# Kernel optimization log

Measured on AMD Instinct MI355X. Metric: run time of the kernel, lower is better.

Reference implementation:

```python
import jax, jax.numpy as jnp
import numpy as np

TAU = 2.0
EPS = 1e-5
SG_ALPHA = 4.0  # spikingjelly default Sigmoid surrogate alpha


@jax.custom_vjp
def heaviside(x):
    return (x >= 0.0).astype(x.dtype)

def _heaviside_fwd(x):
    return heaviside(x), x

def _heaviside_bwd(x, g):
    s = jax.nn.sigmoid(SG_ALPHA * x)
    return (g * SG_ALPHA * s * (1.0 - s),)

heaviside.defvjp(_heaviside_fwd, _heaviside_bwd)


def lif(x_seq, v_th):
    """Multi-step LIF, hard reset to 0, detach_reset=True. x_seq: (T, ...)."""
    def step(v, x_t):
        v = v + (x_t - v) / TAU
        s = heaviside(v - v_th)
        v = v * (1.0 - jax.lax.stop_gradient(s))  # detached hard reset
        return v, s
    _, spikes = jax.lax.scan(step, jnp.zeros_like(x_seq[0]), x_seq)
    return spikes


def bn(y, gamma, beta, mean, var):
    # y: (T, B, C, N); inference-mode BatchNorm1d over channel dim
    inv = gamma / jnp.sqrt(var + EPS)
    return y * inv[None, None, :, None] + (beta - mean * inv)[None, None, :, None]


def setup_inputs() -> dict:
    key = jax.random.key(0)
    ks = jax.random.split(key, 8)
    T, B, C, H, W = 4, 32, 256, 32, 32
    d = {
        "x": jax.random.normal(ks[0], (T, B, C, H, W), jnp.float32),
        "q_w": jax.random.normal(ks[1], (C, C), jnp.float32) * (1.0 / np.sqrt(C)),
        "q_gamma": jnp.ones((C,), jnp.float32),
        "q_beta": jnp.zeros((C,), jnp.float32),
        "q_mean": jnp.zeros((C,), jnp.float32),
        "q_var": jnp.ones((C,), jnp.float32),
        "k_w": jax.random.normal(ks[2], (C, C), jnp.float32) * (1.0 / np.sqrt(C)),
        "k_gamma": jnp.ones((C,), jnp.float32),
        "k_beta": jnp.zeros((C,), jnp.float32),
        "k_mean": jnp.zeros((C,), jnp.float32),
        "k_var": jnp.ones((C,), jnp.float32),
        "p_w": jax.random.normal(ks[3], (C, C), jnp.float32) * (1.0 / np.sqrt(C)),
        "p_b": jnp.zeros((C,), jnp.float32),
        "p_gamma": jnp.ones((C,), jnp.float32),
        "p_beta": jnp.zeros((C,), jnp.float32),
        "p_mean": jnp.zeros((C,), jnp.float32),
        "p_var": jnp.ones((C,), jnp.float32),
    }
    return d


def reference(x, q_w, q_gamma, q_beta, q_mean, q_var,
              k_w, k_gamma, k_beta, k_mean, k_var,
              p_w, p_b, p_gamma, p_beta, p_mean, p_var):
    T, B, C, H, W = x.shape
    num_heads = 8
    dh = C // num_heads
    N = H * W
    xs = x.reshape(T, B, C, N)

    # Q branch: 1x1 conv (C x C matmul) -> BN -> LIF
    q = bn(jnp.einsum('oc,tbcn->tbon', q_w, xs), q_gamma, q_beta, q_mean, q_var)
    q_spikes = lif(q, 1.0)                                # (T,B,C,N)
    q_h = q_spikes.reshape(T, B, num_heads, dh, N)

    # K branch
    k = bn(jnp.einsum('oc,tbcn->tbon', k_w, xs), k_gamma, k_beta, k_mean, k_var)
    k_spikes = lif(k, 1.0)
    k_h = k_spikes.reshape(T, B, num_heads, dh, N)

    # channel-sum pooled Q per head -> attn LIF (v_th=0.5) -> elementwise mult with K
    q_sum = jnp.sum(q_h, axis=3, keepdims=True)           # (T,B,h,1,N)
    attn = lif(q_sum, 0.5)
    x_one = attn * k_h                                    # (T,B,h,dh,N)

    # projection: 1x1 conv with bias -> BN -> LIF
    xo = x_one.reshape(T, B, C, N)
    xo = jnp.einsum('oc,tbcn->tbon', p_w, xo) + p_b[None, None, :, None]
    xo = bn(xo, p_gamma, p_beta, p_mean, p_var).reshape(T, B, C, H, W)
    x_final = lif(xo, 1.0)
    return x_final
```

## Files before the change

kernel.cpp:

```cpp
#include <hip/hip_runtime.h>
#include <cstdint>
#include <cstddef>

#define T_DIM 4
#define B_DIM 32
#define C_DIM 256
#define N_DIM 1024
#define NHEAD 8
#define DHEAD 32
#define NWRD 32

__device__ __forceinline__ float lif_step(float& v, float x, float vth) {
    v = __fadd_rn(v, __fmul_rn(__fsub_rn(x, v), 0.5f));
    const float s = (v >= vth) ? 1.0f : 0.0f;
    if (s != 0.0f) v = 0.0f;
    return s;
}

__device__ __forceinline__ void async_copy16(const float* g, float* l) {
    __builtin_amdgcn_global_load_lds(
        (const __attribute__((address_space(1))) unsigned int*)g,
        (__attribute__((address_space(3))) unsigned int*)l, 16, 0, 0);
}

__global__ __launch_bounds__(256) void k_transpose(
    const float* __restrict__ qw, const float* __restrict__ kw,
    const float* __restrict__ pw, float* __restrict__ wqk_t,
    float* __restrict__ p_t)
{
    const int i = blockIdx.x * 256 + threadIdx.x;
    if (i < C_DIM * 512) {
        const int k = i >> 9, col = i & 511;
        const int h = col >> 6, j = col & 63;
        wqk_t[i] = (j < 32) ? qw[(size_t)(h * 32 + j) * C_DIM + k]
                            : kw[(size_t)(h * 32 + j - 32) * C_DIM + k];
    } else {
        const int i2 = i - C_DIM * 512;
        const int k = i2 >> 8, c = i2 & 255;
        p_t[i2] = pw[(size_t)c * C_DIM + k];
    }
}

__global__ __launch_bounds__(256) void k_qk(
    const float* __restrict__ x, const float* __restrict__ wqk,
    const float* __restrict__ qg, const float* __restrict__ qbeta,
    const float* __restrict__ qmean, const float* __restrict__ qvar,
    const float* __restrict__ kg, const float* __restrict__ kbeta,
    const float* __restrict__ kmean, const float* __restrict__ kvar,
    uint32_t* __restrict__ xbits)
{
    __shared__ float w_lds[64 * 64];
    __shared__ float x_lds[64 * 64];
    __shared__ float qsum_lds[64];
    __shared__ float attn_lds[64];
    __shared__ uint32_t pack_lds[64];

    const int tid = threadIdx.x;
    const int h = blockIdx.x, nt = blockIdx.y, b = blockIdx.z;
    const int n0g = nt * 64;

    const int  mg   = tid >> 4;
    const int  m0   = mg << 2;
    const int  n0   = (tid & 15) << 2;
    const bool is_q = (mg < 8);

    float inv4[4], bias4[4];
    {
        const float* g  = is_q ? qg    : kg;
        const float* be = is_q ? qbeta : kbeta;
        const float* me = is_q ? qmean : kmean;
        const float* va = is_q ? qvar  : kvar;
        const int cb = h * DHEAD + (is_q ? m0 : (m0 - 32));
        #pragma unroll
        for (int i = 0; i < 4; i++) {
            const float iv = __fdiv_rn(g[cb + i], __fsqrt_rn(__fadd_rn(va[cb + i], 1e-5f)));
            inv4[i]  = iv;
            bias4[i] = __fsub_rn(be[cb + i], __fmul_rn(me[cb + i], iv));
        }
    }

    const int wid  = tid >> 6, lane = tid & 63;
    const int lr   = lane >> 4;
    const int lc   = (lane & 15) << 2;
    const int rbase = wid * 16;

    float* wl_dst = w_lds + rbase * 64;
    float* xl_dst = x_lds + rbase * 64;
    const float* wg0 = wqk + (size_t)(rbase + lr) * 512 + h * 64 + lc;

    float vstate[16];
    #pragma unroll
    for (int i = 0; i < 16; i++) vstate[i] = 0.0f;
    float v_attn = 0.0f;

    for (int t = 0; t < T_DIM; ++t) {
        float acc[16];
        #pragma unroll
        for (int i = 0; i < 16; i++) acc[i] = 0.0f;

        const float* xg0 = x + ((size_t)(t * B_DIM + b) * C_DIM + rbase + lr) * N_DIM + n0g + lc;

        for (int kk = 0; kk < C_DIM; kk += 64) {
            #pragma unroll
            for (int i = 0; i < 4; i++) {
                async_copy16(wg0 + (size_t)(kk + i * 4) * 512,   wl_dst + i * 256);
                async_copy16(xg0 + (size_t)(kk + i * 4) * N_DIM, xl_dst + i * 256);
            }
            __syncthreads();
            #pragma unroll 4
            for (int k = 0; k < 64; k++) {
                const float4 a  = *(const float4*)(w_lds + k * 64 + m0);
                const float4 bv = *(const float4*)(x_lds + k * 64 + n0);
                acc[ 0] = fmaf(a.x, bv.x, acc[ 0]);
                acc[ 1] = fmaf(a.x, bv.y, acc[ 1]);
                acc[ 2] = fmaf(a.x, bv.z, acc[ 2]);
                acc[ 3] = fmaf(a.x, bv.w, acc[ 3]);
                acc[ 4] = fmaf(a.y, bv.x, acc[ 4]);
                acc[ 5] = fmaf(a.y, bv.y, acc[ 5]);
                acc[ 6] = fmaf(a.y, bv.z, acc[ 6]);
                acc[ 7] = fmaf(a.y, bv.w, acc[ 7]);
                acc[ 8] = fmaf(a.z, bv.x, acc[ 8]);
                acc[ 9] = fmaf(a.z, bv.y, acc[ 9]);
                acc[10] = fmaf(a.z, bv.z, acc[10]);
                acc[11] = fmaf(a.z, bv.w, acc[11]);
                acc[12] = fmaf(a.w, bv.x, acc[12]);
                acc[13] = fmaf(a.w, bv.y, acc[13]);
                acc[14] = fmaf(a.w, bv.z, acc[14]);
                acc[15] = fmaf(a.w, bv.w, acc[15]);
            }
            __syncthreads();
        }

        float sarr[16];
        #pragma unroll
        for (int i = 0; i < 4; i++) {
            #pragma unroll
            for (int j = 0; j < 4; j++) {
                const float y = __fadd_rn(__fmul_rn(acc[i * 4 + j], inv4[i]), bias4[i]);
                sarr[i * 4 + j] = lif_step(vstate[i * 4 + j], y, 1.0f);
            }
        }

        if (tid < 64) { qsum_lds[tid] = 0.0f; pack_lds[tid] = 0u; }
        __syncthreads();

        if (is_q) {
            #pragma unroll
            for (int j = 0; j < 4; j++) {
                const float cs = sarr[j] + sarr[4 + j] + sarr[8 + j] + sarr[12 + j];
                atomicAdd(&qsum_lds[n0 + j], cs);
            }
        }
        __syncthreads();
        if (tid < 64) attn_lds[tid] = lif_step(v_attn, qsum_lds[tid], 0.5f);
        __syncthreads();

        if (!is_q) {
            #pragma unroll
            for (int i = 0; i < 4; i++) {
                uint32_t nib = 0;
                #pragma unroll
                for (int j = 0; j < 4; j++) {
                    if (sarr[i * 4 + j] != 0.0f && attn_lds[n0 + j] != 0.0f)
                        nib |= (1u << j);
                }
                if (nib)
                    atomicOr(&pack_lds[((m0 - 32) + i) * 2 + (n0 >> 5)], nib << (n0 & 31));
            }
        }
        __syncthreads();
        if (tid < 64) {
            const int row = tid >> 1, word = tid & 1;
            const int c = h * DHEAD + row;
            xbits[((size_t)(t * B_DIM + b) * C_DIM + c) * NWRD + (n0g >> 5) + word] = pack_lds[tid];
        }
    }
}

__global__ __launch_bounds__(256) void k_proj(
    const uint32_t* __restrict__ xbits, const float* __restrict__ pt,
    const float* __restrict__ pbias, const float* __restrict__ pg,
    const float* __restrict__ pbeta, const float* __restrict__ pmean,
    const float* __restrict__ pvar, float* __restrict__ out)
{
    __shared__ float w_lds[64 * 64];
    __shared__ float x_lds[64 * 64];

    const int tid = threadIdx.x;
    const int mt = blockIdx.x, nt = blockIdx.y, b = blockIdx.z;
    const int n0g = nt * 64;
    const int c0  = mt * 64;

    const int mg = tid >> 4, m0 = mg << 2;
    const int n0 = (tid & 15) << 2;

    float inv4[4], bias4[4], pb4[4];
    #pragma unroll
    for (int i = 0; i < 4; i++) {
        const int c = c0 + m0 + i;
        const float iv = __fdiv_rn(pg[c], __fsqrt_rn(__fadd_rn(pvar[c], 1e-5f)));
        inv4[i]  = iv;
        bias4[i] = __fsub_rn(pbeta[c], __fmul_rn(pmean[c], iv));
        pb4[i]   = pbias[c];
    }

    const int wid = tid >> 6, lane = tid & 63;
    const int lr  = lane >> 4;
    const int lc  = (lane & 15) << 2;
    const int rbase = wid * 16;

    float* wl_dst = w_lds + rbase * 64;
    const float* wg0 = pt + (size_t)(rbase + lr) * 256 + c0 + lc;
    const int wsel = (lane & 15) >> 3;
    const int shf  = (lane & 7) * 4;

    float vstate[16];
    #pragma unroll
    for (int i = 0; i < 16; i++) vstate[i] = 0.0f;

    for (int t = 0; t < T_DIM; ++t) {
        float acc[16];
        #pragma unroll
        for (int i = 0; i < 16; i++) acc[i] = 0.0f;

        const uint32_t* xg0 = xbits + ((size_t)(t * B_DIM + b) * C_DIM + rbase + lr) * NWRD
                              + (n0g >> 5) + wsel;

        for (int kk = 0; kk < C_DIM; kk += 64) {
            #pragma unroll
            for (int i = 0; i < 4; i++)
                async_copy16(wg0 + (size_t)(kk + i * 4) * 256, wl_dst + i * 256);
            #pragma unroll
            for (int i = 0; i < 4; i++) {
                const uint32_t wv = xg0[(size_t)(kk + i * 4) * NWRD];
                float4 f;
                f.x = ((wv >> (shf + 0)) & 1u) ? 1.0f : 0.0f;
                f.y = ((wv >> (shf + 1)) & 1u) ? 1.0f : 0.0f;
                f.z = ((wv >> (shf + 2)) & 1u) ? 1.0f : 0.0f;
                f.w = ((wv >> (shf + 3)) & 1u) ? 1.0f : 0.0f;
                *(float4*)(x_lds + (rbase + i * 4 + lr) * 64 + lc) = f;
            }
            __syncthreads();
            #pragma unroll 4
            for (int k = 0; k < 64; k++) {
                const float4 a  = *(const float4*)(w_lds + k * 64 + m0);
                const float4 bv = *(const float4*)(x_lds + k * 64 + n0);
                acc[ 0] = fmaf(a.x, bv.x, acc[ 0]);
                acc[ 1] = fmaf(a.x, bv.y, acc[ 1]);
                acc[ 2] = fmaf(a.x, bv.z, acc[ 2]);
                acc[ 3] = fmaf(a.x, bv.w, acc[ 3]);
                acc[ 4] = fmaf(a.y, bv.x, acc[ 4]);
                acc[ 5] = fmaf(a.y, bv.y, acc[ 5]);
                acc[ 6] = fmaf(a.y, bv.z, acc[ 6]);
                acc[ 7] = fmaf(a.y, bv.w, acc[ 7]);
                acc[ 8] = fmaf(a.z, bv.x, acc[ 8]);
                acc[ 9] = fmaf(a.z, bv.y, acc[ 9]);
                acc[10] = fmaf(a.z, bv.z, acc[10]);
                acc[11] = fmaf(a.z, bv.w, acc[11]);
                acc[12] = fmaf(a.w, bv.x, acc[12]);
                acc[13] = fmaf(a.w, bv.y, acc[13]);
                acc[14] = fmaf(a.w, bv.z, acc[14]);
                acc[15] = fmaf(a.w, bv.w, acc[15]);
            }
            __syncthreads();
        }

        #pragma unroll
        for (int i = 0; i < 4; i++) {
            float s4[4];
            #pragma unroll
            for (int j = 0; j < 4; j++) {
                float y = __fadd_rn(acc[i * 4 + j], pb4[i]);
                y = __fadd_rn(__fmul_rn(y, inv4[i]), bias4[i]);
                s4[j] = lif_step(vstate[i * 4 + j], y, 1.0f);
            }
            const int c = c0 + m0 + i;
            float4 o4;
            o4.x = s4[0]; o4.y = s4[1]; o4.z = s4[2]; o4.w = s4[3];
            *(float4*)(out + ((size_t)(t * B_DIM + b) * C_DIM + c) * N_DIM + n0g + n0) = o4;
        }
    }
}

extern "C" void kernel_launch(void* const* d_in, const int* in_sizes, int n_in,
                              void* d_out, int out_size, void* d_ws, size_t ws_size,
                              hipStream_t stream) {
    const float* x    = (const float*)d_in[0];
    const float* q_w  = (const float*)d_in[1];
    const float* q_g  = (const float*)d_in[2];
    const float* q_b  = (const float*)d_in[3];
    const float* q_m  = (const float*)d_in[4];
    const float* q_v  = (const float*)d_in[5];
    const float* k_w  = (const float*)d_in[6];
    const float* k_g  = (const float*)d_in[7];
    const float* k_b  = (const float*)d_in[8];
    const float* k_m  = (const float*)d_in[9];
    const float* k_v  = (const float*)d_in[10];
    const float* p_w  = (const float*)d_in[11];
    const float* p_b  = (const float*)d_in[12];
    const float* p_g  = (const float*)d_in[13];
    const float* p_be = (const float*)d_in[14];
    const float* p_m  = (const float*)d_in[15];
    const float* p_v  = (const float*)d_in[16];

    float*    wqk_t = (float*)d_ws;
    float*    p_t   = (float*)((char*)d_ws + 524288);
    uint32_t* xbits = (uint32_t*)((char*)d_ws + 786432);
    float*    out   = (float*)d_out;

    k_transpose<<<768, 256, 0, stream>>>(q_w, k_w, p_w, wqk_t, p_t);

    dim3 g1(NHEAD, N_DIM / 64, B_DIM);
    k_qk<<<g1, 256, 0, stream>>>(x, wqk_t, q_g, q_b, q_m, q_v,
                                 k_g, k_b, k_m, k_v, xbits);

    dim3 g2(C_DIM / 64, N_DIM / 64, B_DIM);
    k_proj<<<g2, 256, 0, stream>>>(xbits, p_t, p_b, p_g, p_be, p_m, p_v, out);
}
```

Baseline: 907.3 us.

## Keep full weight slice resident in LDS and double-buffer activation tiles

Both GEMM kernels now load the whole 256x64 weight slice into LDS once per block instead of reloading it for every timestep and K chunk. The activation tiles are double-buffered in 32-row chunks, so the next chunk is fetched while the current one is multiplied, with one barrier per chunk instead of two. This removes repeated weight traffic and hides global load latency. In exchange LDS use rises to about 80 KB per block, which may cut occupancy to one or two blocks per CU, and the scratch arrays for the Q-sum stage now alias the activation buffer, which needs an extra barrier.

```diff
diff --git a/kernel.cpp b/kernel.cpp
--- a/kernel.cpp
+++ b/kernel.cpp
@@ -22,6 +22,24 @@
         (const __attribute__((address_space(1))) unsigned int*)g,
         (__attribute__((address_space(3))) unsigned int*)l, 16, 0, 0);
 }
+
+#define FMA16(a, bv)                          \
+    acc[ 0] = fmaf(a.x, bv.x, acc[ 0]);       \
+    acc[ 1] = fmaf(a.x, bv.y, acc[ 1]);       \
+    acc[ 2] = fmaf(a.x, bv.z, acc[ 2]);       \
+    acc[ 3] = fmaf(a.x, bv.w, acc[ 3]);       \
+    acc[ 4] = fmaf(a.y, bv.x, acc[ 4]);       \
+    acc[ 5] = fmaf(a.y, bv.y, acc[ 5]);       \
+    acc[ 6] = fmaf(a.y, bv.z, acc[ 6]);       \
+    acc[ 7] = fmaf(a.y, bv.w, acc[ 7]);       \
+    acc[ 8] = fmaf(a.z, bv.x, acc[ 8]);       \
+    acc[ 9] = fmaf(a.z, bv.y, acc[ 9]);       \
+    acc[10] = fmaf(a.z, bv.z, acc[10]);       \
+    acc[11] = fmaf(a.z, bv.w, acc[11]);       \
+    acc[12] = fmaf(a.w, bv.x, acc[12]);       \
+    acc[13] = fmaf(a.w, bv.y, acc[13]);       \
+    acc[14] = fmaf(a.w, bv.z, acc[14]);       \
+    acc[15] = fmaf(a.w, bv.w, acc[15]);
 
 __global__ __launch_bounds__(256) void k_transpose(
     const float* __restrict__ qw, const float* __restrict__ kw,
@@ -49,11 +67,11 @@
     const float* __restrict__ kmean, const float* __restrict__ kvar,
     uint32_t* __restrict__ xbits)
 {
-    __shared__ float w_lds[64 * 64];
-    __shared__ float x_lds[64 * 64];
-    __shared__ float qsum_lds[64];
-    __shared__ float attn_lds[64];
-    __shared__ uint32_t pack_lds[64];
+    __shared__ float w_lds[C_DIM * 64];
+    __shared__ float x_lds[2][32 * 64];
+    float*    qsum_lds = &x_lds[0][0];
+    float*    attn_lds = &x_lds[0][64];
+    uint32_t* pack_lds = (uint32_t*)&x_lds[0][128];
 
     const int tid = threadIdx.x;
     const int h = blockIdx.x, nt = blockIdx.y, b = blockIdx.z;
@@ -79,14 +97,17 @@
         }
     }
 
-    const int wid  = tid >> 6, lane = tid & 63;
-    const int lr   = lane >> 4;
-    const int lc   = (lane & 15) << 2;
-    const int rbase = wid * 16;
-
-    float* wl_dst = w_lds + rbase * 64;
-    float* xl_dst = x_lds + rbase * 64;
-    const float* wg0 = wqk + (size_t)(rbase + lr) * 512 + h * 64 + lc;
+    const int wid = tid >> 6, lane = tid & 63;
+    const int lr  = lane >> 4;
+    const int lc  = (lane & 15) << 2;
+
+    {
+        const float* wg = wqk + (size_t)(wid * 64 + lr) * 512 + h * 64 + lc;
+        float* wl = w_lds + (size_t)(wid * 64) * 64;
+        #pragma unroll
+        for (int j = 0; j < 16; j++)
+            async_copy16(wg + (size_t)(j * 4) * 512, wl + j * 256);
+    }
 
     float vstate[16];
     #pragma unroll
@@ -98,37 +119,28 @@
         #pragma unroll
         for (int i = 0; i < 16; i++) acc[i] = 0.0f;
 
-        const float* xg0 = x + ((size_t)(t * B_DIM + b) * C_DIM + rbase + lr) * N_DIM + n0g + lc;
-
-        for (int kk = 0; kk < C_DIM; kk += 64) {
-            #pragma unroll
-            for (int i = 0; i < 4; i++) {
-                async_copy16(wg0 + (size_t)(kk + i * 4) * 512,   wl_dst + i * 256);
-                async_copy16(xg0 + (size_t)(kk + i * 4) * N_DIM, xl_dst + i * 256);
-            }
+        const float* xg = x + ((size_t)(t * B_DIM + b) * C_DIM + wid * 8 + lr) * N_DIM
+                          + n0g + lc;
+
+        async_copy16(xg,                       x_lds[0] + wid * 512);
+        async_copy16(xg + (size_t)4 * N_DIM,   x_lds[0] + wid * 512 + 256);
+
+        for (int c = 0; c < 8; ++c) {
             __syncthreads();
+            if (c + 1 < 8) {
+                const size_t ko = (size_t)((c + 1) * 32);
+                float* dst = x_lds[(c + 1) & 1] + wid * 512;
+                async_copy16(xg + (ko    ) * N_DIM, dst);
+                async_copy16(xg + (ko + 4) * N_DIM, dst + 256);
+            }
+            const float* xl = x_lds[c & 1];
+            const float* wl = w_lds + (size_t)(c * 32) * 64;
             #pragma unroll 4
-            for (int k = 0; k < 64; k++) {
-                const float4 a  = *(const float4*)(w_lds + k * 64 + m0);
-                const float4 bv = *(const float4*)(x_lds + k * 64 + n0);
-                acc[ 0] = fmaf(a.x, bv.x, acc[ 0]);
-                acc[ 1] = fmaf(a.x, bv.y, acc[ 1]);
-                acc[ 2] = fmaf(a.x, bv.z, acc[ 2]);
-                acc[ 3] = fmaf(a.x, bv.w, acc[ 3]);
-                acc[ 4] = fmaf(a.y, bv.x, acc[ 4]);
-                acc[ 5] = fmaf(a.y, bv.y, acc[ 5]);
-                acc[ 6] = fmaf(a.y, bv.z, acc[ 6]);
-                acc[ 7] = fmaf(a.y, bv.w, acc[ 7]);
-                acc[ 8] = fmaf(a.z, bv.x, acc[ 8]);
-                acc[ 9] = fmaf(a.z, bv.y, acc[ 9]);
-                acc[10] = fmaf(a.z, bv.z, acc[10]);
-                acc[11] = fmaf(a.z, bv.w, acc[11]);
-                acc[12] = fmaf(a.w, bv.x, acc[12]);
-                acc[13] = fmaf(a.w, bv.y, acc[13]);
-                acc[14] = fmaf(a.w, bv.z, acc[14]);
-                acc[15] = fmaf(a.w, bv.w, acc[15]);
-            }
-            __syncthreads();
+            for (int k = 0; k < 32; k++) {
+                const float4 a  = *(const float4*)(wl + k * 64 + m0);
+                const float4 bv = *(const float4*)(xl + k * 64 + n0);
+                FMA16(a, bv)
+            }
         }
 
         float sarr[16];
@@ -172,8 +184,10 @@
         if (tid < 64) {
             const int row = tid >> 1, word = tid & 1;
             const int c = h * DHEAD + row;
-            xbits[((size_t)(t * B_DIM + b) * C_DIM + c) * NWRD + (n0g >> 5) + word] = pack_lds[tid];
-        }
+            xbits[((size_t)(t * B_DIM + b) * C_DIM + c) * NWRD + (n0g >> 5) + word]
+                = pack_lds[tid];
+        }
+        __syncthreads();
     }
 }
 
@@ -183,8 +197,8 @@
     const float* __restrict__ pbeta, const float* __restrict__ pmean,
     const float* __restrict__ pvar, float* __restrict__ out)
 {
-    __shared__ float w_lds[64 * 64];
-    __shared__ float x_lds[64 * 64];
+    __shared__ float w_lds[C_DIM * 64];
+    __shared__ float x_lds[2][32 * 64];
 
     const int tid = threadIdx.x;
     const int mt = blockIdx.x, nt = blockIdx.y, b = blockIdx.z;
@@ -207,12 +221,19 @@
     const int wid = tid >> 6, lane = tid & 63;
     const int lr  = lane >> 4;
     const int lc  = (lane & 15) << 2;
-    const int rbase = wid * 16;
-
-    float* wl_dst = w_lds + rbase * 64;
-    const float* wg0 = pt + (size_t)(rbase + lr) * 256 + c0 + lc;
-    const int wsel = (lane & 15) >> 3;
-    const int shf  = (lane & 7) * 4;
+
+    {
+        const float* wg = pt + (size_t)(wid * 64 + lr) * 256 + c0 + lc;
+        float* wl = w_lds + (size_t)(wid * 64) * 64;
+        #pragma unroll
+        for (int j = 0; j < 16; j++)
+            async_copy16(wg + (size_t)(j * 4) * 256, wl + j * 256);
+    }
+
+    const int r  = tid >> 3, gg = tid & 7;
+    const int shf = (gg & 3) * 8;
+    float* xw0 = &x_lds[0][r * 64 + gg * 8];
+    float* xw1 = &x_lds[1][r * 64 + gg * 8];
 
     float vstate[16];
     #pragma unroll
@@ -223,46 +244,52 @@
         #pragma unroll
         for (int i = 0; i < 16; i++) acc[i] = 0.0f;
 
-        const uint32_t* xg0 = xbits + ((size_t)(t * B_DIM + b) * C_DIM + rbase + lr) * NWRD
-                              + (n0g >> 5) + wsel;
-
-        for (int kk = 0; kk < C_DIM; kk += 64) {
-            #pragma unroll
-            for (int i = 0; i < 4; i++)
-                async_copy16(wg0 + (size_t)(kk + i * 4) * 256, wl_dst + i * 256);
-            #pragma unroll
-            for (int i = 0; i < 4; i++) {
-                const uint32_t wv = xg0[(size_t)(kk + i * 4) * NWRD];
-                float4 f;
-                f.x = ((wv >> (shf + 0)) & 1u) ? 1.0f : 0.0f;
-                f.y = ((wv >> (shf + 1)) & 1u) ? 1.0f : 0.0f;
-                f.z = ((wv >> (shf + 2)) & 1u) ? 1.0f : 0.0f;
-                f.w = ((wv >> (shf + 3)) & 1u) ? 1.0f : 0.0f;
-                *(float4*)(x_lds + (rbase + i * 4 + lr) * 64 + lc) = f;
-            }
+        const uint32_t* xg = xbits + ((size_t)(t * B_DIM + b) * C_DIM + r) * NWRD
+                             + (n0g >> 5) + (gg >> 2);
+
+        uint32_t u = xg[0];
+        {
+            const uint32_t bits = (u >> shf) & 0xffu;
+            float4 f0, f1;
+            f0.x = (bits & 1u)        ? 1.0f : 0.0f;
+            f0.y = ((bits >> 1) & 1u) ? 1.0f : 0.0f;
+            f0.z = ((bits >> 2) & 1u) ? 1.0f : 0.0f;
+            f0.w = ((bits >> 3) & 1u) ? 1.0f : 0.0f;
+            f1.x = ((bits >> 4) & 1u) ? 1.0f : 0.0f;
+            f1.y = ((bits >> 5) & 1u) ? 1.0f : 0.0f;
+            f1.z = ((bits >> 6) & 1u) ? 1.0f : 0.0f;
+            f1.w = ((bits >> 7) & 1u) ? 1.0f : 0.0f;
+            *(float4*)xw0       = f0;
+            *(float4*)(xw0 + 4) = f1;
+        }
+        u = xg[(size_t)32 * NWRD];
+
+        for (int c = 0; c < 8; ++c) {
             __syncthreads();
+            if (c + 1 < 8) {
+                const uint32_t bits = (u >> shf) & 0xffu;
+                float4 f0, f1;
+                f0.x = (bits & 1u)        ? 1.0f : 0.0f;
+                f0.y = ((bits >> 1) & 1u) ? 1.0f : 0.0f;
+                f0.z = ((bits >> 2) & 1u) ? 1.0f : 0.0f;
+                f0.w = ((bits >> 3) & 1u) ? 1.0f : 0.0f;
+                f1.x = ((bits >> 4) & 1u) ? 1.0f : 0.0f;
+                f1.y = ((bits >> 5) & 1u) ? 1.0f : 0.0f;
+                f1.z = ((bits >> 6) & 1u) ? 1.0f : 0.0f;
+                f1.w = ((bits >> 7) & 1u) ? 1.0f : 0.0f;
+                float* xw = ((c + 1) & 1) ? xw1 : xw0;
+                *(float4*)xw       = f0;
+                *(float4*)(xw + 4) = f1;
+                if (c + 2 < 8) u = xg[(size_t)(c + 2) * 32 * NWRD];
+            }
+            const float* xl = x_lds[c & 1];
+            const float* wl = w_lds + (size_t)(c * 32) * 64;
             #pragma unroll 4
-            for (int k = 0; k < 64; k++) {
-                const float4 a  = *(const float4*)(w_lds + k * 64 + m0);
-                const float4 bv = *(const float4*)(x_lds + k * 64 + n0);
-                acc[ 0] = fmaf(a.x, bv.x, acc[ 0]);
-                acc[ 1] = fmaf(a.x, bv.y, acc[ 1]);
-                acc[ 2] = fmaf(a.x, bv.z, acc[ 2]);
-                acc[ 3] = fmaf(a.x, bv.w, acc[ 3]);
-                acc[ 4] = fmaf(a.y, bv.x, acc[ 4]);
-                acc[ 5] = fmaf(a.y, bv.y, acc[ 5]);
-                acc[ 6] = fmaf(a.y, bv.z, acc[ 6]);
-                acc[ 7] = fmaf(a.y, bv.w, acc[ 7]);
-                acc[ 8] = fmaf(a.z, bv.x, acc[ 8]);
-                acc[ 9] = fmaf(a.z, bv.y, acc[ 9]);
-                acc[10] = fmaf(a.z, bv.z, acc[10]);
-                acc[11] = fmaf(a.z, bv.w, acc[11]);
-                acc[12] = fmaf(a.w, bv.x, acc[12]);
-                acc[13] = fmaf(a.w, bv.y, acc[13]);
-                acc[14] = fmaf(a.w, bv.z, acc[14]);
-                acc[15] = fmaf(a.w, bv.w, acc[15]);
-            }
-            __syncthreads();
+            for (int k = 0; k < 32; k++) {
+                const float4 a  = *(const float4*)(wl + k * 64 + m0);
+                const float4 bv = *(const float4*)(xl + k * 64 + n0);
+                FMA16(a, bv)
+            }
         }
 
         #pragma unroll
```

Result: slower. 1.022 ms (+12.7%).

## Widen GEMM tiles to 64x128 with 4x8 per-thread micro-tiles and 32-deep K chunks

Applied to the files above, without the earlier changes.

Both the QK and projection kernels now compute 64x128 output tiles per block, with each thread holding a 4x8 accumulator tile instead of 4x4. The K loop is split into 32-deep chunks, and the trailing barrier moves to the start of each chunk. The projection kernel prefetches the next chunk's packed spike bits into registers during compute. This raises arithmetic intensity per LDS read and halves the grid size, at the cost of more registers (occupancy hint 4), fewer blocks, and shared memory reused for the qsum, attn and pack buffers.

```diff
diff --git a/kernel.cpp b/kernel.cpp
--- a/kernel.cpp
+++ b/kernel.cpp
@@ -22,6 +22,16 @@
         (const __attribute__((address_space(1))) unsigned int*)g,
         (__attribute__((address_space(3))) unsigned int*)l, 16, 0, 0);
 }
+
+#define FMA_ROW(r, av)                                \
+    acc[(r)*8+0] = fmaf(av, b0.x, acc[(r)*8+0]);      \
+    acc[(r)*8+1] = fmaf(av, b0.y, acc[(r)*8+1]);      \
+    acc[(r)*8+2] = fmaf(av, b0.z, acc[(r)*8+2]);      \
+    acc[(r)*8+3] = fmaf(av, b0.w, acc[(r)*8+3]);      \
+    acc[(r)*8+4] = fmaf(av, b1.x, acc[(r)*8+4]);      \
+    acc[(r)*8+5] = fmaf(av, b1.y, acc[(r)*8+5]);      \
+    acc[(r)*8+6] = fmaf(av, b1.z, acc[(r)*8+6]);      \
+    acc[(r)*8+7] = fmaf(av, b1.w, acc[(r)*8+7]);
 
 __global__ __launch_bounds__(256) void k_transpose(
     const float* __restrict__ qw, const float* __restrict__ kw,
@@ -41,7 +51,7 @@
     }
 }
 
-__global__ __launch_bounds__(256) void k_qk(
+__global__ __launch_bounds__(256, 4) void k_qk(
     const float* __restrict__ x, const float* __restrict__ wqk,
     const float* __restrict__ qg, const float* __restrict__ qbeta,
     const float* __restrict__ qmean, const float* __restrict__ qvar,
@@ -49,19 +59,20 @@
     const float* __restrict__ kmean, const float* __restrict__ kvar,
     uint32_t* __restrict__ xbits)
 {
-    __shared__ float w_lds[64 * 64];
-    __shared__ float x_lds[64 * 64];
-    __shared__ float qsum_lds[64];
-    __shared__ float attn_lds[64];
-    __shared__ uint32_t pack_lds[64];
+    __shared__ float w_lds[32 * 64];
+    __shared__ float x_lds[32 * 128];
+    float*    qsum_lds = x_lds;
+    float*    attn_lds = x_lds + 128;
+    uint32_t* pack_lds = (uint32_t*)(x_lds + 256);
 
     const int tid = threadIdx.x;
     const int h = blockIdx.x, nt = blockIdx.y, b = blockIdx.z;
-    const int n0g = nt * 64;
-
-    const int  mg   = tid >> 4;
-    const int  m0   = mg << 2;
-    const int  n0   = (tid & 15) << 2;
+    const int n0g = nt * 128;
+
+    const int  mg = tid >> 4;
+    const int  m0 = mg << 2;
+    const int  ng = tid & 15;
+    const int  n0 = ng << 2;
     const bool is_q = (mg < 8);
 
     float inv4[4], bias4[4];
@@ -79,205 +90,202 @@
         }
     }
 
-    const int wid  = tid >> 6, lane = tid & 63;
-    const int lr   = lane >> 4;
-    const int lc   = (lane & 15) << 2;
-    const int rbase = wid * 16;
-
-    float* wl_dst = w_lds + rbase * 64;
-    float* xl_dst = x_lds + rbase * 64;
-    const float* wg0 = wqk + (size_t)(rbase + lr) * 512 + h * 64 + lc;
-
-    float vstate[16];
+    const int wk = tid >> 4;
+    const int wm = (tid & 15) << 2;
+    const int xk = tid >> 5;
+    const int xc = (tid & 31) << 2;
+    const float* wgp = wqk + h * 64 + wm;
+
+    float vstate[32];
     #pragma unroll
-    for (int i = 0; i < 16; i++) vstate[i] = 0.0f;
+    for (int i = 0; i < 32; i++) vstate[i] = 0.0f;
     float v_attn = 0.0f;
 
     for (int t = 0; t < T_DIM; ++t) {
-        float acc[16];
-        #pragma unroll
-        for (int i = 0; i < 16; i++) acc[i] = 0.0f;
-
-        const float* xg0 = x + ((size_t)(t * B_DIM + b) * C_DIM + rbase + lr) * N_DIM + n0g + lc;
-
-        for (int kk = 0; kk < C_DIM; kk += 64) {
-            #pragma unroll
-            for (int i = 0; i < 4; i++) {
-                async_copy16(wg0 + (size_t)(kk + i * 4) * 512,   wl_dst + i * 256);
-                async_copy16(xg0 + (size_t)(kk + i * 4) * N_DIM, xl_dst + i * 256);
-            }
+        float acc[32];
+        #pragma unroll
+        for (int i = 0; i < 32; i++) acc[i] = 0.0f;
+
+        const float* xgp = x + (size_t)(t * B_DIM + b) * C_DIM * N_DIM + n0g + xc;
+
+        for (int c = 0; c < 8; ++c) {
+            const int kk = c * 32;
+            __syncthreads();
+            async_copy16(wgp + (size_t)(kk      + wk) * 512, w_lds + tid * 4);
+            async_copy16(wgp + (size_t)(kk + 16 + wk) * 512, w_lds + 1024 + tid * 4);
+            #pragma unroll
+            for (int r = 0; r < 4; r++)
+                async_copy16(xgp + (size_t)(kk + r * 8 + xk) * N_DIM,
+                             x_lds + r * 1024 + tid * 4);
             __syncthreads();
             #pragma unroll 4
-            for (int k = 0; k < 64; k++) {
+            for (int k = 0; k < 32; k++) {
                 const float4 a  = *(const float4*)(w_lds + k * 64 + m0);
-                const float4 bv = *(const float4*)(x_lds + k * 64 + n0);
-                acc[ 0] = fmaf(a.x, bv.x, acc[ 0]);
-                acc[ 1] = fmaf(a.x, bv.y, acc[ 1]);
-                acc[ 2] = fmaf(a.x, bv.z, acc[ 2]);
-                acc[ 3] = fmaf(a.x, bv.w, acc[ 3]);
-                acc[ 4] = fmaf(a.y, bv.x, acc[ 4]);
-                acc[ 5] = fmaf(a.y, bv.y, acc[ 5]);
-                acc[ 6] = fmaf(a.y, bv.z, acc[ 6]);
-                acc[ 7] = fmaf(a.y, bv.w, acc[ 7]);
-                acc[ 8] = fmaf(a.z, bv.x, acc[ 8]);
-                acc[ 9] = fmaf(a.z, bv.y, acc[ 9]);
-                acc[10] = fmaf(a.z, bv.z, acc[10]);
-                acc[11] = fmaf(a.z, bv.w, acc[11]);
-                acc[12] = fmaf(a.w, bv.x, acc[12]);
-                acc[13] = fmaf(a.w, bv.y, acc[13]);
-                acc[14] = fmaf(a.w, bv.z, acc[14]);
-                acc[15] = fmaf(a.w, bv.w, acc[15]);
-            }
-            __syncthreads();
-        }
-
-        float sarr[16];
-        #pragma unroll
-        for (int i = 0; i < 4; i++) {
-            #pragma unroll
-            for (int j = 0; j < 4; j++) {
-                const float y = __fadd_rn(__fmul_rn(acc[i * 4 + j], inv4[i]), bias4[i]);
-                sarr[i * 4 + j] = lif_step(vstate[i * 4 + j], y, 1.0f);
-            }
-        }
-
-        if (tid < 64) { qsum_lds[tid] = 0.0f; pack_lds[tid] = 0u; }
+                const float4 b0 = *(const float4*)(x_lds + k * 128 + n0);
+                const float4 b1 = *(const float4*)(x_lds + k * 128 + 64 + n0);
+                FMA_ROW(0, a.x)
+                FMA_ROW(1, a.y)
+                FMA_ROW(2, a.z)
+                FMA_ROW(3, a.w)
+            }
+        }
+
+        #pragma unroll
+        for (int r = 0; r < 4; r++) {
+            #pragma unroll
+            for (int j = 0; j < 8; j++) {
+                const float y = __fadd_rn(__fmul_rn(acc[r * 8 + j], inv4[r]), bias4[r]);
+                acc[r * 8 + j] = lif_step(vstate[r * 8 + j], y, 1.0f);
+            }
+        }
+
+        __syncthreads();
+        if (tid < 128) qsum_lds[tid] = 0.0f; else pack_lds[tid - 128] = 0u;
         __syncthreads();
 
         if (is_q) {
             #pragma unroll
-            for (int j = 0; j < 4; j++) {
-                const float cs = sarr[j] + sarr[4 + j] + sarr[8 + j] + sarr[12 + j];
-                atomicAdd(&qsum_lds[n0 + j], cs);
-            }
-        }
-        __syncthreads();
-        if (tid < 64) attn_lds[tid] = lif_step(v_attn, qsum_lds[tid], 0.5f);
+            for (int j = 0; j < 8; j++) {
+                const int col = (j < 4) ? (n0 + j) : (64 + n0 + (j - 4));
+                const float cs = acc[j] + acc[8 + j] + acc[16 + j] + acc[24 + j];
+                atomicAdd(&qsum_lds[col], cs);
+            }
+        }
+        __syncthreads();
+        if (tid < 128) attn_lds[tid] = lif_step(v_attn, qsum_lds[tid], 0.5f);
         __syncthreads();
 
         if (!is_q) {
             #pragma unroll
-            for (int i = 0; i < 4; i++) {
-                uint32_t nib = 0;
+            for (int r = 0; r < 4; r++) {
+                const int krow = (mg - 8) * 4 + r;
                 #pragma unroll
-                for (int j = 0; j < 4; j++) {
-                    if (sarr[i * 4 + j] != 0.0f && attn_lds[n0 + j] != 0.0f)
-                        nib |= (1u << j);
+                for (int ci = 0; ci < 2; ci++) {
+                    uint32_t nib = 0;
+                    #pragma unroll
+                    for (int jj = 0; jj < 4; jj++) {
+                        const int col = ci * 64 + n0 + jj;
+                        if (acc[r * 8 + ci * 4 + jj] != 0.0f && attn_lds[col] != 0.0f)
+                            nib |= (1u << jj);
+                    }
+                    if (nib) {
+                        const int word = ci * 2 + (ng >> 3);
+                        const int shf  = (ng & 7) * 4;
+                        atomicOr(&pack_lds[krow * 4 + word], nib << shf);
+                    }
                 }
-                if (nib)
-                    atomicOr(&pack_lds[((m0 - 32) + i) * 2 + (n0 >> 5)], nib << (n0 & 31));
-            }
-        }
-        __syncthreads();
-        if (tid < 64) {
-            const int row = tid >> 1, word = tid & 1;
-            const int c = h * DHEAD + row;
-            xbits[((size_t)(t * B_DIM + b) * C_DIM + c) * NWRD + (n0g >> 5) + word] = pack_lds[tid];
-        }
-    }
-}
-
-__global__ __launch_bounds__(256) void k_proj(
+            }
+        }
+        __syncthreads();
+        if (tid < 128) {
+            const int krow = tid >> 2, word = tid & 3;
+            const int ch = h * DHEAD + krow;
+            xbits[((size_t)(t * B_DIM + b) * C_DIM + ch) * NWRD + nt * 4 + word]
+                = pack_lds[tid];
+        }
+    }
+}
+
+__global__ __launch_bounds__(256, 4) void k_proj(
     const uint32_t* __restrict__ xbits, const float* __restrict__ pt,
     const float* __restrict__ pbias, const float* __restrict__ pg,
     const float* __restrict__ pbeta, const float* __restrict__ pmean,
     const float* __restrict__ pvar, float* __restrict__ out)
 {
-    __shared__ float w_lds[64 * 64];
-    __shared__ float x_lds[64 * 64];
+    __shared__ float w_lds[32 * 64];
+    __shared__ float x_lds[32 * 128];
 
     const int tid = threadIdx.x;
     const int mt = blockIdx.x, nt = blockIdx.y, b = blockIdx.z;
-    const int n0g = nt * 64;
+    const int n0g = nt * 128;
     const int c0  = mt * 64;
 
     const int mg = tid >> 4, m0 = mg << 2;
-    const int n0 = (tid & 15) << 2;
+    const int ng = tid & 15, n0 = ng << 2;
 
     float inv4[4], bias4[4], pb4[4];
     #pragma unroll
     for (int i = 0; i < 4; i++) {
-        const int c = c0 + m0 + i;
-        const float iv = __fdiv_rn(pg[c], __fsqrt_rn(__fadd_rn(pvar[c], 1e-5f)));
+        const int ch = c0 + m0 + i;
+        const float iv = __fdiv_rn(pg[ch], __fsqrt_rn(__fadd_rn(pvar[ch], 1e-5f)));
         inv4[i]  = iv;
-        bias4[i] = __fsub_rn(pbeta[c], __fmul_rn(pmean[c], iv));
-        pb4[i]   = pbias[c];
-    }
-
-    const int wid = tid >> 6, lane = tid & 63;
-    const int lr  = lane >> 4;
-    const int lc  = (lane & 15) << 2;
-    const int rbase = wid * 16;
-
-    float* wl_dst = w_lds + rbase * 64;
-    const float* wg0 = pt + (size_t)(rbase + lr) * 256 + c0 + lc;
-    const int wsel = (lane & 15) >> 3;
-    const int shf  = (lane & 7) * 4;
-
-    float vstate[16];
+        bias4[i] = __fsub_rn(pbeta[ch], __fmul_rn(pmean[ch], iv));
+        pb4[i]   = pbias[ch];
+    }
+
+    const int wk = tid >> 4;
+    const int wm = (tid & 15) << 2;
+    const float* wgp = pt + c0 + wm;
+
+    const int usel = nt * 4 + ((tid & 31) >> 3);
+    const int shf  = (tid & 7) * 4;
+    const int urow = tid >> 5;
+
+    float vstate[32];
     #pragma unroll
-    for (int i = 0; i < 16; i++) vstate[i] = 0.0f;
+    for (int i = 0; i < 32; i++) vstate[i] = 0.0f;
 
     for (int t = 0; t < T_DIM; ++t) {
-        float acc[16];
-        #pragma unroll
-        for (int i = 0; i < 16; i++) acc[i] = 0.0f;
-
-        const uint32_t* xg0 = xbits + ((size_t)(t * B_DIM + b) * C_DIM + rbase + lr) * NWRD
-                              + (n0g >> 5) + wsel;
-
-        for (int kk = 0; kk < C_DIM; kk += 64) {
-            #pragma unroll
-            for (int i = 0; i < 4; i++)
-                async_copy16(wg0 + (size_t)(kk + i * 4) * 256, wl_dst + i * 256);
-            #pragma unroll
-            for (int i = 0; i < 4; i++) {
-                const uint32_t wv = xg0[(size_t)(kk + i * 4) * NWRD];
+        float acc[32];
+        #pragma unroll
+        for (int i = 0; i < 32; i++) acc[i] = 0.0f;
+
+        const uint32_t* xg = xbits + (size_t)(t * B_DIM + b) * C_DIM * NWRD;
+
+        uint32_t u[4];
+        #pragma unroll
+        for (int r = 0; r < 4; r++)
+            u[r] = xg[(size_t)(r * 8 + urow) * NWRD + usel];
+
+        for (int c = 0; c < 8; ++c) {
+            __syncthreads();
+            #pragma unroll
+            for (int r = 0; r < 4; r++) {
+                const uint32_t bits = (u[r] >> shf) & 0xFu;
                 float4 f;
-                f.x = ((wv >> (shf + 0)) & 1u) ? 1.0f : 0.0f;
-                f.y = ((wv >> (shf + 1)) & 1u) ? 1.0f : 0.0f;
-                f.z = ((wv >> (shf + 2)) & 1u) ? 1.0f : 0.0f;
-                f.w = ((wv >> (shf + 3)) & 1u) ? 1.0f : 0.0f;
-                *(float4*)(x_lds + (rbase + i * 4 + lr) * 64 + lc) = f;
-            }
+                f.x = (bits & 1u)        ? 1.0f : 0.0f;
+                f.y = ((bits >> 1) & 1u) ? 1.0f : 0.0f;
+                f.z = ((bits >> 2) & 1u) ? 1.0f : 0.0f;
+                f.w = ((bits >> 3) & 1u) ? 1.0f : 0.0f;
+                *(float4*)(x_lds + r * 1024 + tid * 4) = f;
+            }
+            async_copy16(wgp + (size_t)(c * 32      + wk) * 256, w_lds + tid * 4);
+            async_copy16(wgp + (size_t)(c * 32 + 16 + wk) * 256, w_lds + 1024 + tid * 4);
             __syncthreads();
+            if (c + 1 < 8) {
+                #pragma unroll
+                for (int r = 0; r < 4; r++)
+                    u[r] = xg[(size_t)((c + 1) * 32 + r * 8 + urow) * NWRD + usel];
+            }
             #pragma unroll 4
-            for (int k = 0; k < 64; k++) {
+            for (int k = 0; k < 32; k++) {
                 const float4 a  = *(const float4*)(w_lds + k * 64 + m0);
-                const float4 bv = *(const float4*)(x_lds + k * 64 + n0);
-                acc[ 0] = fmaf(a.x, bv.x, acc[ 0]);
-                acc[ 1] = fmaf(a.x, bv.y, acc[ 1]);
-                acc[ 2] = fmaf(a.x, bv.z, acc[ 2]);
-                acc[ 3] = fmaf(a.x, bv.w, acc[ 3]);
-                acc[ 4] = fmaf(a.y, bv.x, acc[ 4]);
-                acc[ 5] = fmaf(a.y, bv.y, acc[ 5]);
-                acc[ 6] = fmaf(a.y, bv.z, acc[ 6]);
-                acc[ 7] = fmaf(a.y, bv.w, acc[ 7]);
-                acc[ 8] = fmaf(a.z, bv.x, acc[ 8]);
-                acc[ 9] = fmaf(a.z, bv.y, acc[ 9]);
-                acc[10] = fmaf(a.z, bv.z, acc[10]);
-                acc[11] = fmaf(a.z, bv.w, acc[11]);
-                acc[12] = fmaf(a.w, bv.x, acc[12]);
-                acc[13] = fmaf(a.w, bv.y, acc[13]);
-                acc[14] = fmaf(a.w, bv.z, acc[14]);
-                acc[15] = fmaf(a.w, bv.w, acc[15]);
-            }
-            __syncthreads();
-        }
-
-        #pragma unroll
-        for (int i = 0; i < 4; i++) {
-            float s4[4];
-            #pragma unroll
-            for (int j = 0; j < 4; j++) {
-                float y = __fadd_rn(acc[i * 4 + j], pb4[i]);
-                y = __fadd_rn(__fmul_rn(y, inv4[i]), bias4[i]);
-                s4[j] = lif_step(vstate[i * 4 + j], y, 1.0f);
-            }
-            const int c = c0 + m0 + i;
-            float4 o4;
-            o4.x = s4[0]; o4.y = s4[1]; o4.z = s4[2]; o4.w = s4[3];
-            *(float4*)(out + ((size_t)(t * B_DIM + b) * C_DIM + c) * N_DIM + n0g + n0) = o4;
+                const float4 b0 = *(const float4*)(x_lds + k * 128 + n0);
+                const float4 b1 = *(const float4*)(x_lds + k * 128 + 64 + n0);
+                FMA_ROW(0, a.x)
+                FMA_ROW(1, a.y)
+                FMA_ROW(2, a.z)
+                FMA_ROW(3, a.w)
+            }
+        }
+
+        #pragma unroll
+        for (int r = 0; r < 4; r++) {
+            const int ch = c0 + m0 + r;
+            float* ob = out + ((size_t)(t * B_DIM + b) * C_DIM + ch) * N_DIM + n0g;
+            float4 oA, oB;
+            float oAv[4], oBv[4];
+            #pragma unroll
+            for (int j = 0; j < 8; j++) {
+                float y = __fadd_rn(acc[r * 8 + j], pb4[r]);
+                y = __fadd_rn(__fmul_rn(y, inv4[r]), bias4[r]);
+                const float s = lif_step(vstate[r * 8 + j], y, 1.0f);
+                if (j < 4) oAv[j] = s; else oBv[j - 4] = s;
+            }
+            oA.x = oAv[0]; oA.y = oAv[1]; oA.z = oAv[2]; oA.w = oAv[3];
+            oB.x = oBv[0]; oB.y = oBv[1]; oB.z = oBv[2]; oB.w = oBv[3];
+            *(float4*)(ob + n0)      = oA;
+            *(float4*)(ob + 64 + n0) = oB;
         }
     }
 }
@@ -310,10 +318,10 @@
 
     k_transpose<<<768, 256, 0, stream>>>(q_w, k_w, p_w, wqk_t, p_t);
 
-    dim3 g1(NHEAD, N_DIM / 64, B_DIM);
+    dim3 g1(NHEAD, N_DIM / 128, B_DIM);
     k_qk<<<g1, 256, 0, stream>>>(x, wqk_t, q_g, q_b, q_m, q_v,
                                  k_g, k_b, k_m, k_v, xbits);
 
-    dim3 g2(C_DIM / 64, N_DIM / 64, B_DIM);
+    dim3 g2(C_DIM / 64, N_DIM / 128, B_DIM);
     k_proj<<<g2, 256, 0, stream>>>(xbits, p_t, p_b, p_g, p_be, p_m, p_v, out);
 }
```

Result: faster. 877.6 us (-3.3%).
